# Optimization experiments

Hardware: AMD Instinct MI355X
Metric: run time of the kernel (lower is better)

Reference implementation:

```python
import jax, jax.numpy as jnp
import numpy as np

N_NODES = 100000
N_EDGES = 3200000
D_IN = 128
D_OUT = 128


def setup_inputs() -> dict:
    key = jax.random.key(0)
    k1, k2, k3, k4, k5, k6 = jax.random.split(key, 6)
    x = jax.random.normal(k1, (N_NODES, D_IN), dtype=jnp.float32)
    edge_row = jnp.sort(jax.random.randint(k2, (N_EDGES,), 0, N_NODES, dtype=jnp.int32))
    edge_col = jax.random.randint(k3, (N_EDGES,), 0, N_NODES, dtype=jnp.int32)
    edge_val = jax.random.uniform(k4, (N_EDGES,), dtype=jnp.float32)
    stdv = 1.0 / np.sqrt(D_OUT)
    weight = jax.random.uniform(k5, (D_IN, D_OUT), dtype=jnp.float32, minval=-stdv, maxval=stdv)
    bias = jax.random.uniform(k6, (D_OUT,), dtype=jnp.float32, minval=-stdv, maxval=stdv)
    return {"x": x, "edge_row": edge_row, "edge_col": edge_col,
            "edge_val": edge_val, "weight": weight, "bias": bias}


def reference(x, edge_row, edge_col, edge_val, weight, bias):
    # support = A @ x  (sparse COO SpMM via gather + segment-sum scatter)
    gathered = x[edge_col] * edge_val[:, None]          # [E, D_IN]
    support = jax.ops.segment_sum(gathered, edge_row, num_segments=N_NODES)  # [N, D_IN]
    # output = support @ W + b
    return support @ weight + bias
```

## Files before the change

kernel.cpp:

```cpp
#include <hip/hip_runtime.h>

#define NNODES 100000
#define NEDGES 3200000
#define DIM    128

typedef __bf16  bf16x8 __attribute__((ext_vector_type(8)));
typedef unsigned short u16;
typedef u16     u16x8  __attribute__((ext_vector_type(8)));
typedef float   f32x4  __attribute__((ext_vector_type(4)));
typedef unsigned int u32;
typedef u32     u32x4  __attribute__((ext_vector_type(4)));

__device__ __forceinline__ u16 bfbits(float f) {
    __bf16 h = (__bf16)f;
    return __builtin_bit_cast(u16, h);
}

__device__ __forceinline__ float asf(u32 u) {
    union { u32 i; float f; } c; c.i = u; return c.f;
}

__device__ __forceinline__ bf16x8 ldfrag_u16(const u16* p) {
    u16x8 u = *(const u16x8*)p;
    return __builtin_bit_cast(bf16x8, u);
}

__device__ __forceinline__ bf16x8 cvt8(f32x4 a, f32x4 b) {
    bf16x8 r;
#pragma unroll
    for (int i = 0; i < 4; ++i) {
        r[i]     = (__bf16)a[i];
        r[4 + i] = (__bf16)b[i];
    }
    return r;
}

__global__ void prep(const int* __restrict__ edge_row, int* __restrict__ row_ptr,
                     const float* __restrict__ w, u16* __restrict__ wt) {
    int gid = blockIdx.x * blockDim.x + threadIdx.x;
    if (gid <= NNODES) {
        int lo = 0, hi = NEDGES;
        while (lo < hi) {
            int mid = (lo + hi) >> 1;
            if (edge_row[mid] < gid) lo = mid + 1; else hi = mid;
        }
        row_ptr[gid] = lo;
    }
    if (gid < DIM * DIM) {
        int k = gid >> 7, n = gid & 127;
        wt[n * DIM + k] = bfbits(w[k * DIM + n]);
    }
}

#define WT_STRIDE 136
__global__ __launch_bounds__(256, 4) void gemm_xw(const float* __restrict__ x,
                                                  const u16* __restrict__ wt,
                                                  u16* __restrict__ y) {
    __shared__ u16 wlds[DIM * WT_STRIDE];

    int tid = threadIdx.x;
    {
        const f32x4* src = (const f32x4*)wt;
#pragma unroll
        for (int i = 0; i < 8; ++i) {
            int ci  = tid + 256 * i;
            int row = ci >> 4, off = ci & 15;
            *((f32x4*)(wlds + row * WT_STRIDE) + off) = src[ci];
        }
    }
    __syncthreads();

    int wave = __builtin_amdgcn_readfirstlane(tid >> 6);
    int lane = tid & 63;
    int quad = lane >> 4, l16 = lane & 15;
    int mBase = (blockIdx.x * 4 + wave) * 16;
    int active = (mBase < NNODES);

    const float* xrow = x + (size_t)(mBase + l16) * DIM + quad * 8;

    f32x4 xa[4], xb[4];
    if (active) {
#pragma unroll
        for (int kb = 0; kb < 4; ++kb) {
            xa[kb] = *(const f32x4*)(xrow + kb * 32);
            xb[kb] = *(const f32x4*)(xrow + kb * 32 + 4);
        }
    }

    f32x4 acc[8];
#pragma unroll
    for (int nt = 0; nt < 8; ++nt) acc[nt] = (f32x4){0.f, 0.f, 0.f, 0.f};

    if (active) {
#pragma unroll
        for (int kb = 0; kb < 4; ++kb) {
            bf16x8 a = cvt8(xa[kb], xb[kb]);
#pragma unroll
            for (int nt = 0; nt < 8; ++nt) {
                bf16x8 b = ldfrag_u16(wlds + (nt * 16 + l16) * WT_STRIDE + kb * 32 + quad * 8);
                acc[nt] = __builtin_amdgcn_mfma_f32_16x16x32_bf16(a, b, acc[nt], 0, 0, 0);
            }
        }
    }

    __syncthreads();

    if (active) {
        u16* yb = wlds + wave * (16 * DIM);
#pragma unroll
        for (int nt = 0; nt < 8; ++nt) {
            int col = nt * 16 + l16;
#pragma unroll
            for (int r = 0; r < 4; ++r)
                yb[(quad * 4 + r) * DIM + col] = bfbits(acc[nt][r]);
        }
#pragma unroll
        for (int j = 0; j < 4; ++j) {
            int lr = j * 4 + quad;
            u16x8 t = *(const u16x8*)(yb + lr * DIM + l16 * 8);
            __builtin_nontemporal_store(t, (u16x8*)(y + (size_t)(mBase + lr) * DIM + l16 * 8));
        }
    }
}

__global__ __launch_bounds__(256, 8) void spmm(const int* __restrict__ row_ptr,
                                               const int* __restrict__ ecol,
                                               const float* __restrict__ eval,
                                               const u16* __restrict__ y,
                                               const float* __restrict__ bias,
                                               float* __restrict__ out,
                                               int rowBase) {
    int lane = threadIdx.x & 63;
    int row  = __builtin_amdgcn_readfirstlane(rowBase + blockIdx.x * 4 + (threadIdx.x >> 6));
    if (row >= NNODES) return;

    int lo = row_ptr[row];
    int hi = row_ptr[row + 1];

    int grp = lane >> 4;
    int sub = lane & 15;

    float acc[8];
#pragma unroll
    for (int j = 0; j < 8; ++j) acc[j] = 0.f;

    const u16* ychunk = y + sub * 8;

    int e = lo;
    for (; e + 16 <= hi; e += 16) {
#pragma unroll
        for (int b = 0; b < 4; ++b) {
            int e0 = e + b * 4;
            int   c0 = ecol[e0], c1 = ecol[e0 + 1], c2 = ecol[e0 + 2], c3 = ecol[e0 + 3];
            float v0 = eval[e0], v1 = eval[e0 + 1], v2 = eval[e0 + 2], v3 = eval[e0 + 3];
            int   c = grp < 2 ? (grp == 0 ? c0 : c1) : (grp == 2 ? c2 : c3);
            float v = grp < 2 ? (grp == 0 ? v0 : v1) : (grp == 2 ? v2 : v3);
            u32x4 q = *(const u32x4*)(ychunk + (size_t)c * DIM);
#pragma unroll
            for (int j = 0; j < 4; ++j) {
                acc[2 * j]     += v * asf(q[j] << 16);
                acc[2 * j + 1] += v * asf(q[j] & 0xffff0000u);
            }
        }
    }
    for (; e < hi; e += 4) {
        int rem = hi - e;
        int i1 = rem > 1 ? e + 1 : e, i2 = rem > 2 ? e + 2 : e, i3 = rem > 3 ? e + 3 : e;
        int   c0 = ecol[e],  c1 = ecol[i1], c2 = ecol[i2], c3 = ecol[i3];
        float v0 = eval[e];
        float v1 = rem > 1 ? eval[i1] : 0.f;
        float v2 = rem > 2 ? eval[i2] : 0.f;
        float v3 = rem > 3 ? eval[i3] : 0.f;
        int   c = grp < 2 ? (grp == 0 ? c0 : c1) : (grp == 2 ? c2 : c3);
        float v = grp < 2 ? (grp == 0 ? v0 : v1) : (grp == 2 ? v2 : v3);
        u32x4 q = *(const u32x4*)(ychunk + (size_t)c * DIM);
#pragma unroll
        for (int j = 0; j < 4; ++j) {
            acc[2 * j]     += v * asf(q[j] << 16);
            acc[2 * j + 1] += v * asf(q[j] & 0xffff0000u);
        }
    }

#pragma unroll
    for (int j = 0; j < 8; ++j) {
        acc[j] += __shfl_xor(acc[j], 16);
        acc[j] += __shfl_xor(acc[j], 32);
    }

    if (grp == 0) {
        float* orow = out + (size_t)row * DIM + sub * 8;
        f32x4 o0, o1;
#pragma unroll
        for (int j = 0; j < 4; ++j) {
            o0[j] = acc[j]     + bias[sub * 8 + j];
            o1[j] = acc[4 + j] + bias[sub * 8 + 4 + j];
        }
        __builtin_nontemporal_store(o0, (f32x4*)orow);
        __builtin_nontemporal_store(o1, (f32x4*)(orow + 4));
    }
}

extern "C" void kernel_launch(void* const* d_in, const int* in_sizes, int n_in,
                              void* d_out, int out_size, void* d_ws, size_t ws_size,
                              hipStream_t stream) {
    const float* x        = (const float*)d_in[0];
    const int*   edge_row = (const int*)d_in[1];
    const int*   edge_col = (const int*)d_in[2];
    const float* edge_val = (const float*)d_in[3];
    const float* weight   = (const float*)d_in[4];
    const float* bias     = (const float*)d_in[5];
    float* out = (float*)d_out;

    char* ws = (char*)d_ws;
    u16* y       = (u16*)ws;
    int* row_ptr = (int*)(ws + (size_t)NNODES * DIM * 2);
    u16* wt      = (u16*)(ws + 26000128);

    prep<<<(NNODES + 1 + 255) / 256, 256, 0, stream>>>(edge_row, row_ptr, weight, wt);

    gemm_xw<<<(NNODES / 16 + 3) / 4, 256, 0, stream>>>(x, wt, y);

    spmm<<<NNODES / 8, 256, 0, stream>>>(row_ptr, edge_col, edge_val, y, bias, out, 0);
    spmm<<<NNODES / 8, 256, 0, stream>>>(row_ptr, edge_col, edge_val, y, bias, out, NNODES / 2);
}
```

Before: 252.7 us.

## Process two row tiles per wave in GEMM and merge SpMM launches

The GEMM kernel now has each wave compute two 16-row tiles, so every LDS weight fragment feeds two MFMAs. The x loads are issued before the barrier so they overlap with the weight staging into LDS, and out-of-range rows are clamped instead of branched on. The two half-size SpMM launches are merged into one full-grid launch, removing a launch boundary. The change costs more registers per wave, which lowers the occupancy bound from 4 to 3.

```diff
diff --git a/kernel.cpp b/kernel.cpp
--- a/kernel.cpp
+++ b/kernel.cpp
@@ -53,7 +53,7 @@
 }
 
 #define WT_STRIDE 136
-__global__ __launch_bounds__(256, 4) void gemm_xw(const float* __restrict__ x,
+__global__ __launch_bounds__(256, 3) void gemm_xw(const float* __restrict__ x,
                                                   const u16* __restrict__ wt,
                                                   u16* __restrict__ y) {
     __shared__ u16 wlds[DIM * WT_STRIDE];
@@ -68,57 +68,74 @@
             *((f32x4*)(wlds + row * WT_STRIDE) + off) = src[ci];
         }
     }
-    __syncthreads();
 
     int wave = __builtin_amdgcn_readfirstlane(tid >> 6);
     int lane = tid & 63;
     int quad = lane >> 4, l16 = lane & 15;
-    int mBase = (blockIdx.x * 4 + wave) * 16;
-    int active = (mBase < NNODES);
-
-    const float* xrow = x + (size_t)(mBase + l16) * DIM + quad * 8;
-
-    f32x4 xa[4], xb[4];
-    if (active) {
-#pragma unroll
-        for (int kb = 0; kb < 4; ++kb) {
-            xa[kb] = *(const f32x4*)(xrow + kb * 32);
-            xb[kb] = *(const f32x4*)(xrow + kb * 32 + 4);
-        }
-    }
-
-    f32x4 acc[8];
-#pragma unroll
-    for (int nt = 0; nt < 8; ++nt) acc[nt] = (f32x4){0.f, 0.f, 0.f, 0.f};
-
-    if (active) {
-#pragma unroll
-        for (int kb = 0; kb < 4; ++kb) {
-            bf16x8 a = cvt8(xa[kb], xb[kb]);
-#pragma unroll
-            for (int nt = 0; nt < 8; ++nt) {
-                bf16x8 b = ldfrag_u16(wlds + (nt * 16 + l16) * WT_STRIDE + kb * 32 + quad * 8);
-                acc[nt] = __builtin_amdgcn_mfma_f32_16x16x32_bf16(a, b, acc[nt], 0, 0, 0);
-            }
-        }
+    int mBase = (blockIdx.x * 8 + wave * 2) * 16;
+
+    int r0 = mBase + l16;      if (r0 >= NNODES) r0 = NNODES - 1;
+    int r1 = mBase + 16 + l16; if (r1 >= NNODES) r1 = NNODES - 1;
+    const float* x0 = x + (size_t)r0 * DIM + quad * 8;
+    const float* x1 = x + (size_t)r1 * DIM + quad * 8;
+
+    f32x4 t0a[4], t0b[4], t1a[4], t1b[4];
+#pragma unroll
+    for (int kb = 0; kb < 4; ++kb) {
+        t0a[kb] = *(const f32x4*)(x0 + kb * 32);
+        t0b[kb] = *(const f32x4*)(x0 + kb * 32 + 4);
+    }
+#pragma unroll
+    for (int kb = 0; kb < 4; ++kb) {
+        t1a[kb] = *(const f32x4*)(x1 + kb * 32);
+        t1b[kb] = *(const f32x4*)(x1 + kb * 32 + 4);
+    }
+    bf16x8 a0[4], a1[4];
+#pragma unroll
+    for (int kb = 0; kb < 4; ++kb) {
+        a0[kb] = cvt8(t0a[kb], t0b[kb]);
+        a1[kb] = cvt8(t1a[kb], t1b[kb]);
     }
 
     __syncthreads();
 
-    if (active) {
-        u16* yb = wlds + wave * (16 * DIM);
+    f32x4 acc0[8], acc1[8];
+#pragma unroll
+    for (int nt = 0; nt < 8; ++nt) {
+        acc0[nt] = (f32x4){0.f, 0.f, 0.f, 0.f};
+        acc1[nt] = (f32x4){0.f, 0.f, 0.f, 0.f};
+    }
+
+#pragma unroll
+    for (int kb = 0; kb < 4; ++kb) {
+#pragma unroll
+        for (int nt = 0; nt < 8; ++nt) {
+            bf16x8 b = ldfrag_u16(wlds + (nt * 16 + l16) * WT_STRIDE + kb * 32 + quad * 8);
+            acc0[nt] = __builtin_amdgcn_mfma_f32_16x16x32_bf16(a0[kb], b, acc0[nt], 0, 0, 0);
+            acc1[nt] = __builtin_amdgcn_mfma_f32_16x16x32_bf16(a1[kb], b, acc1[nt], 0, 0, 0);
+        }
+    }
+
+    __syncthreads();
+
+    {
+        u16* yb = wlds + wave * (32 * DIM);
 #pragma unroll
         for (int nt = 0; nt < 8; ++nt) {
             int col = nt * 16 + l16;
 #pragma unroll
-            for (int r = 0; r < 4; ++r)
-                yb[(quad * 4 + r) * DIM + col] = bfbits(acc[nt][r]);
-        }
-#pragma unroll
-        for (int j = 0; j < 4; ++j) {
+            for (int r = 0; r < 4; ++r) {
+                yb[(quad * 4 + r) * DIM + col]        = bfbits(acc0[nt][r]);
+                yb[(16 + quad * 4 + r) * DIM + col]   = bfbits(acc1[nt][r]);
+            }
+        }
+#pragma unroll
+        for (int j = 0; j < 8; ++j) {
             int lr = j * 4 + quad;
-            u16x8 t = *(const u16x8*)(yb + lr * DIM + l16 * 8);
-            __builtin_nontemporal_store(t, (u16x8*)(y + (size_t)(mBase + lr) * DIM + l16 * 8));
+            if (mBase + lr < NNODES) {
+                u16x8 t = *(const u16x8*)(yb + lr * DIM + l16 * 8);
+                __builtin_nontemporal_store(t, (u16x8*)(y + (size_t)(mBase + lr) * DIM + l16 * 8));
+            }
         }
     }
 }
@@ -128,10 +145,9 @@
                                                const float* __restrict__ eval,
                                                const u16* __restrict__ y,
                                                const float* __restrict__ bias,
-                                               float* __restrict__ out,
-                                               int rowBase) {
+                                               float* __restrict__ out) {
     int lane = threadIdx.x & 63;
-    int row  = __builtin_amdgcn_readfirstlane(rowBase + blockIdx.x * 4 + (threadIdx.x >> 6));
+    int row  = __builtin_amdgcn_readfirstlane(blockIdx.x * 4 + (threadIdx.x >> 6));
     if (row >= NNODES) return;
 
     int lo = row_ptr[row];
@@ -218,8 +234,7 @@
 
     prep<<<(NNODES + 1 + 255) / 256, 256, 0, stream>>>(edge_row, row_ptr, weight, wt);
 
-    gemm_xw<<<(NNODES / 16 + 3) / 4, 256, 0, stream>>>(x, wt, y);
-
-    spmm<<<NNODES / 8, 256, 0, stream>>>(row_ptr, edge_col, edge_val, y, bias, out, 0);
-    spmm<<<NNODES / 8, 256, 0, stream>>>(row_ptr, edge_col, edge_val, y, bias, out, NNODES / 2);
-}
+    gemm_xw<<<(NNODES + 127) / 128, 256, 0, stream>>>(x, wt, y);
+
+    spmm<<<NNODES / 4, 256, 0, stream>>>(row_ptr, edge_col, edge_val, y, bias, out);
+}
```

Measured after the change: 248.8 us (median of 2 runs). No clear change (-1.5%).
